# Kernel tuning notes

Hardware: AMD Instinct MI355X
Metric: run time of the kernel (lower is better)

Reference implementation:

```python
import jax, jax.numpy as jnp
import numpy as np


def setup_inputs() -> dict:
    key = jax.random.key(0)
    ks = jax.random.split(key, 16)
    s = 0.02
    return {
        "video": jax.random.normal(ks[0], (256, 10, 7, 7, 512), jnp.float32),
        "audio": jax.random.normal(ks[1], (10, 256, 128), jnp.float32),
        "Wv1": jax.random.normal(ks[2], (512, 512), jnp.float32) * s,
        "bv1": jnp.zeros((512,), jnp.float32),
        "Wa1": jax.random.normal(ks[3], (512, 128), jnp.float32) * s,
        "ba1": jnp.zeros((512,), jnp.float32),
        "Wb": jax.random.normal(ks[4], (256, 512), jnp.float32) * s,
        "bb": jnp.zeros((256,), jnp.float32),
        "Wc": jax.random.normal(ks[5], (512, 256), jnp.float32) * s,
        "bc": jnp.zeros((512,), jnp.float32),
        "Wv2": jax.random.normal(ks[6], (256, 512), jnp.float32) * s,
        "bv2": jnp.zeros((256,), jnp.float32),
        "Wa2": jax.random.normal(ks[7], (256, 128), jnp.float32) * s,
        "ba2": jnp.zeros((256,), jnp.float32),
        "Ws": jax.random.normal(ks[8], (1, 256), jnp.float32) * s,
        "bs": jnp.zeros((1,), jnp.float32),
    }


def reference(video, audio, Wv1, bv1, Wa1, ba1, Wb, bb, Wc, bc, Wv2, bv2, Wa2, ba2, Ws, bs):
    # video: [B, T, H, W, 512]; audio: [T, B, 128] (transposed inside, as in torch code)
    relu = jax.nn.relu
    audio = jnp.transpose(audio, (1, 0, 2))                  # [B, T, 128]
    B, T, H, W, Vd = video.shape
    BT, HW = B * T, H * W
    af = audio.reshape(BT, -1)                               # [BT, 128]
    vf = video.reshape(B, T, HW, Vd)                         # raw visual feature

    # channel attention
    aq1 = relu(af @ Wa1.T + ba1)[:, None, :]                 # [BT, 1, 512]
    vq1 = relu(vf @ Wv1.T + bv1).reshape(BT, HW, -1)         # [BT, 49, 512]
    avq = jnp.mean(aq1 * vq1, axis=-2)                       # [BT, 512]
    avq = relu(avq @ Wb.T + bb)                              # [BT, 256]
    c_att_maps = jax.nn.sigmoid(avq @ Wc.T + bc).reshape(B, T, 1, Vd)
    c_att = (vf * (c_att_maps + 1.0)).reshape(BT, HW, Vd)    # [BT, 49, 512]

    # spatial attention
    cq = relu(c_att @ Wv2.T + bv2)                           # [BT, 49, 256]
    aq2 = relu(af @ Wa2.T + ba2)[:, None, :]                 # [BT, 1, 256]
    logits = jnp.tanh((cq * aq2) @ Ws.T + bs)                # [BT, 49, 1]
    s_att = jax.nn.softmax(jnp.transpose(logits, (0, 2, 1)), axis=-1)  # [BT, 1, 49]

    out = jnp.matmul(s_att, c_att)                           # [BT, 1, 512]
    return out.reshape(B, T, Vd)
```

## Files before the change

### kernel.cpp

```cpp
#include <hip/hip_runtime.h>

typedef __bf16 bf16x8 __attribute__((ext_vector_type(8)));
typedef float f32x4 __attribute__((ext_vector_type(4)));

__device__ __forceinline__ unsigned short f2bf(float f) {
    union { float f; unsigned int u; } x; x.f = f;
    unsigned int r = x.u + 0x7FFFu + ((x.u >> 16) & 1u);
    return (unsigned short)(r >> 16);
}
__device__ __forceinline__ float bf2f(unsigned short v) {
    union { unsigned int u; float f; } x; x.u = ((unsigned int)v) << 16; return x.f;
}

__global__ __launch_bounds__(256) void k_prep(
    const float* __restrict__ Wv1, const float* __restrict__ Wv2,
    unsigned short* __restrict__ Wv1bf, unsigned short* __restrict__ Wv2bf)
{
    int idx = blockIdx.x * 256 + threadIdx.x;
    if (idx < 262144) {
        Wv1bf[idx] = f2bf(Wv1[idx]);
    } else {
        int j = idx - 262144;
        Wv2bf[j] = f2bf(Wv2[j]);
    }
}

__global__ __launch_bounds__(256) void k_audio(
    const float* __restrict__ audio,
    const float* __restrict__ Wa1, const float* __restrict__ ba1,
    const float* __restrict__ Wa2, const float* __restrict__ ba2,
    float* __restrict__ aq1, float* __restrict__ aq2)
{
    __shared__ float afs[4][128];
    const int btBase = blockIdx.x * 4;
    const int tid = threadIdx.x;
    for (int i = tid; i < 512; i += 256) {
        int g = i >> 7, k = i & 127;
        int bt = btBase + g;
        int b = bt / 10, t = bt - b * 10;
        afs[g][k] = audio[(t * 256 + b) * 128 + k];
    }
    __syncthreads();
    const int c = tid;
    float a1a[4] = {0.f,0.f,0.f,0.f}, a1b[4] = {0.f,0.f,0.f,0.f}, a2[4] = {0.f,0.f,0.f,0.f};
    const float* w1a = Wa1 + c * 128;
    const float* w1b = Wa1 + (c + 256) * 128;
    const float* w2p = Wa2 + c * 128;
    for (int kk = 0; kk < 32; ++kk) {
        float4 va = *(const float4*)(w1a + kk * 4);
        float4 vb = *(const float4*)(w1b + kk * 4);
        float4 vc = *(const float4*)(w2p + kk * 4);
        float fa[4] = {va.x, va.y, va.z, va.w};
        float fb[4] = {vb.x, vb.y, vb.z, vb.w};
        float fc[4] = {vc.x, vc.y, vc.z, vc.w};
#pragma unroll
        for (int j = 0; j < 4; ++j) {
            int k = kk * 4 + j;
#pragma unroll
            for (int g = 0; g < 4; ++g) {
                float a = afs[g][k];
                a1a[g] += a * fa[j];
                a1b[g] += a * fb[j];
                a2[g]  += a * fc[j];
            }
        }
    }
    float b1a = ba1[c], b1b = ba1[c + 256], b2 = ba2[c];
#pragma unroll
    for (int g = 0; g < 4; ++g) {
        int bt = btBase + g;
        aq1[bt * 512 + c]       = fmaxf(a1a[g] + b1a, 0.f);
        aq1[bt * 512 + c + 256] = fmaxf(a1b[g] + b1b, 0.f);
        aq2[bt * 256 + c]       = fmaxf(a2[g] + b2, 0.f);
    }
}

__global__ __launch_bounds__(256) void k_chanatt(
    const float* __restrict__ video,
    const unsigned short* __restrict__ Wv1bf, const float* __restrict__ bv1,
    const float* __restrict__ aq1, float* __restrict__ avq)
{
    __shared__ unsigned short At[49 * 512];
    const int bt = blockIdx.x;
    const int tid = threadIdx.x;
    const int wave = tid >> 6, lane = tid & 63, quad = lane >> 4, l16 = lane & 15;
    const float* vsrc = video + (size_t)bt * 25088;

    for (int c = tid; c < 3136; c += 256) {
        int row = c >> 6, ch = c & 63;
        float4 a = *(const float4*)(vsrc + row * 512 + ch * 8);
        float4 b = *(const float4*)(vsrc + row * 512 + ch * 8 + 4);
        float f[8] = {a.x, a.y, a.z, a.w, b.x, b.y, b.z, b.w};
        unsigned int o[8];
#pragma unroll
        for (int j = 0; j < 8; ++j) o[j] = f2bf(f[j]);
        uint4 pack;
        pack.x = o[0] | (o[1] << 16); pack.y = o[2] | (o[3] << 16);
        pack.z = o[4] | (o[5] << 16); pack.w = o[6] | (o[7] << 16);
        int chs = ch ^ (row & 7);
        *(uint4*)(&At[row * 512 + chs * 8]) = pack;
    }
    __syncthreads();

    f32x4 acc[4][8];
#pragma unroll
    for (int mt = 0; mt < 4; ++mt)
#pragma unroll
        for (int nt = 0; nt < 8; ++nt)
            acc[mt][nt] = (f32x4){0.f, 0.f, 0.f, 0.f};

    for (int kk = 0; kk < 16; ++kk) {
        int chunk = kk * 4 + quad;
        bf16x8 afrag[4];
#pragma unroll
        for (int mt = 0; mt < 4; ++mt) {
            int m = ((mt == 3) ? 33 : mt * 16) + l16;
            int chs = chunk ^ (m & 7);
            afrag[mt] = *(const bf16x8*)(&At[m * 512 + chs * 8]);
        }
        int koff = chunk * 8;
#pragma unroll
        for (int nt = 0; nt < 8; ++nt) {
            int n = (wave * 8 + nt) * 16 + l16;
            bf16x8 bfrag = *(const bf16x8*)(Wv1bf + n * 512 + koff);
#pragma unroll
            for (int mt = 0; mt < 4; ++mt)
                acc[mt][nt] = __builtin_amdgcn_mfma_f32_16x16x32_bf16(
                    afrag[mt], bfrag, acc[mt][nt], 0, 0, 0);
        }
    }

#pragma unroll
    for (int nt = 0; nt < 8; ++nt) {
        int n = (wave * 8 + nt) * 16 + l16;
        float bias = bv1[n];
        float s = 0.f;
#pragma unroll
        for (int mt = 0; mt < 4; ++mt)
#pragma unroll
            for (int r = 0; r < 4; ++r)
                if (mt < 3 || (quad == 3 && r == 3))
                    s += fmaxf(acc[mt][nt][r] + bias, 0.f);
        s += __shfl_xor(s, 16, 64);
        s += __shfl_xor(s, 32, 64);
        if (quad == 0) {
            float vm = s * (1.f / 49.f);
            avq[bt * 512 + n] = aq1[bt * 512 + n] * vm;
        }
    }
}

__global__ __launch_bounds__(256) void k_mlp(
    const float* __restrict__ avq,
    const float* __restrict__ Wb, const float* __restrict__ bb,
    const float* __restrict__ Wc, const float* __restrict__ bc,
    float* __restrict__ cmul)
{
    __shared__ float av[4][512];
    __shared__ float hid[4][256];
    const int btBase = blockIdx.x * 4;
    const int tid = threadIdx.x;
    for (int i = tid; i < 2048; i += 256) {
        int g = i >> 9, c = i & 511;
        av[g][c] = avq[(btBase + g) * 512 + c];
    }
    __syncthreads();
    {
        float a[4] = {0.f,0.f,0.f,0.f};
        const float* wrow = Wb + tid * 512;
        for (int kk = 0; kk < 128; ++kk) {
            float4 v = *(const float4*)(wrow + kk * 4);
            float w[4] = {v.x, v.y, v.z, v.w};
#pragma unroll
            for (int j = 0; j < 4; ++j)
#pragma unroll
                for (int g = 0; g < 4; ++g)
                    a[g] += av[g][kk * 4 + j] * w[j];
        }
        float bias = bb[tid];
#pragma unroll
        for (int g = 0; g < 4; ++g) hid[g][tid] = fmaxf(a[g] + bias, 0.f);
    }
    __syncthreads();
#pragma unroll
    for (int rep = 0; rep < 2; ++rep) {
        int c = tid + rep * 256;
        float a[4] = {0.f,0.f,0.f,0.f};
        const float* wrow = Wc + c * 256;
        for (int kk = 0; kk < 64; ++kk) {
            float4 v = *(const float4*)(wrow + kk * 4);
            float w[4] = {v.x, v.y, v.z, v.w};
#pragma unroll
            for (int j = 0; j < 4; ++j)
#pragma unroll
                for (int g = 0; g < 4; ++g)
                    a[g] += hid[g][kk * 4 + j] * w[j];
        }
        float bias = bc[c];
#pragma unroll
        for (int g = 0; g < 4; ++g) {
            float s = 1.f / (1.f + __expf(-(a[g] + bias)));
            cmul[(btBase + g) * 512 + c] = 1.f + s;
        }
    }
}

__global__ __launch_bounds__(256) void k_spatial(
    const float* __restrict__ video,
    const float* __restrict__ cmul, const float* __restrict__ aq2,
    const unsigned short* __restrict__ Wv2bf, const float* __restrict__ bv2,
    const float* __restrict__ Wsp, const float* __restrict__ bsp,
    float* __restrict__ out)
{
    __shared__ unsigned short Ct[49 * 512];
    __shared__ float w2[256];
    __shared__ float zbuf[4][64];
    __shared__ float smw[64];
    const int bt = blockIdx.x;
    const int tid = threadIdx.x;
    const int wave = tid >> 6, lane = tid & 63, quad = lane >> 4, l16 = lane & 15;
    const float* vsrc = video + (size_t)bt * 25088;
    const float* cm = cmul + bt * 512;

    for (int c = tid; c < 3136; c += 256) {
        int row = c >> 6, ch = c & 63;
        float4 a = *(const float4*)(vsrc + row * 512 + ch * 8);
        float4 b = *(const float4*)(vsrc + row * 512 + ch * 8 + 4);
        float f[8] = {a.x, a.y, a.z, a.w, b.x, b.y, b.z, b.w};
        float4 m0 = *(const float4*)(cm + ch * 8);
        float4 m1 = *(const float4*)(cm + ch * 8 + 4);
        float mm[8] = {m0.x, m0.y, m0.z, m0.w, m1.x, m1.y, m1.z, m1.w};
        unsigned int o[8];
#pragma unroll
        for (int j = 0; j < 8; ++j) o[j] = f2bf(f[j] * mm[j]);
        uint4 pack;
        pack.x = o[0] | (o[1] << 16); pack.y = o[2] | (o[3] << 16);
        pack.z = o[4] | (o[5] << 16); pack.w = o[6] | (o[7] << 16);
        int chs = ch ^ (row & 7);
        *(uint4*)(&Ct[row * 512 + chs * 8]) = pack;
    }
    w2[tid] = aq2[bt * 256 + tid] * Wsp[tid];
    if (lane >= 49) zbuf[wave][lane] = 0.f;
    __syncthreads();

    f32x4 acc[4][4];
#pragma unroll
    for (int mt = 0; mt < 4; ++mt)
#pragma unroll
        for (int nt = 0; nt < 4; ++nt)
            acc[mt][nt] = (f32x4){0.f, 0.f, 0.f, 0.f};

    for (int kk = 0; kk < 16; ++kk) {
        int chunk = kk * 4 + quad;
        bf16x8 afrag[4];
#pragma unroll
        for (int mt = 0; mt < 4; ++mt) {
            int m = ((mt == 3) ? 33 : mt * 16) + l16;
            int chs = chunk ^ (m & 7);
            afrag[mt] = *(const bf16x8*)(&Ct[m * 512 + chs * 8]);
        }
        int koff = chunk * 8;
#pragma unroll
        for (int nt = 0; nt < 4; ++nt) {
            int n = (wave * 4 + nt) * 16 + l16;
            bf16x8 bfrag = *(const bf16x8*)(Wv2bf + n * 512 + koff);
#pragma unroll
            for (int mt = 0; mt < 4; ++mt)
                acc[mt][nt] = __builtin_amdgcn_mfma_f32_16x16x32_bf16(
                    afrag[mt], bfrag, acc[mt][nt], 0, 0, 0);
        }
    }

    float zp[16];
#pragma unroll
    for (int i = 0; i < 16; ++i) zp[i] = 0.f;
#pragma unroll
    for (int nt = 0; nt < 4; ++nt) {
        int n = (wave * 4 + nt) * 16 + l16;
        float bias = bv2[n];
        float wn = w2[n];
#pragma unroll
        for (int mt = 0; mt < 4; ++mt)
#pragma unroll
            for (int r = 0; r < 4; ++r)
                zp[mt * 4 + r] += fmaxf(acc[mt][nt][r] + bias, 0.f) * wn;
    }
#pragma unroll
    for (int i = 0; i < 16; ++i) {
        float v = zp[i];
        v += __shfl_xor(v, 1, 64);
        v += __shfl_xor(v, 2, 64);
        v += __shfl_xor(v, 4, 64);
        v += __shfl_xor(v, 8, 64);
        zp[i] = v;
    }
    if (l16 == 0) {
#pragma unroll
        for (int mt = 0; mt < 4; ++mt)
#pragma unroll
            for (int r = 0; r < 4; ++r)
                if (mt < 3 || (quad == 3 && r == 3)) {
                    int row = ((mt == 3) ? 33 : mt * 16) + quad * 4 + r;
                    zbuf[wave][row] = zp[mt * 4 + r];
                }
    }
    __syncthreads();

    if (wave == 0) {
        int hw = lane;
        float z = zbuf[0][hw] + zbuf[1][hw] + zbuf[2][hw] + zbuf[3][hw] + bsp[0];
        float t = tanhf(z);
        float v = (hw < 49) ? t : -1e30f;
#pragma unroll
        for (int off = 32; off; off >>= 1) v = fmaxf(v, __shfl_xor(v, off, 64));
        float e = (hw < 49) ? __expf(t - v) : 0.f;
        float se = e;
#pragma unroll
        for (int off = 32; off; off >>= 1) se += __shfl_xor(se, off, 64);
        smw[hw] = e / se;
    }
    __syncthreads();

#pragma unroll
    for (int rep = 0; rep < 2; ++rep) {
        int cidx = tid + rep * 256;
        int chb = cidx >> 3, jj = cidx & 7;
        float s = 0.f;
        for (int hw = 0; hw < 49; ++hw) {
            int chs = chb ^ (hw & 7);
            s += smw[hw] * bf2f(Ct[hw * 512 + chs * 8 + jj]);
        }
        out[bt * 512 + cidx] = s;
    }
}

extern "C" void kernel_launch(void* const* d_in, const int* in_sizes, int n_in,
                              void* d_out, int out_size, void* d_ws, size_t ws_size,
                              hipStream_t stream) {
    const float* video = (const float*)d_in[0];
    const float* audio = (const float*)d_in[1];
    const float* Wv1 = (const float*)d_in[2];
    const float* bv1 = (const float*)d_in[3];
    const float* Wa1 = (const float*)d_in[4];
    const float* ba1 = (const float*)d_in[5];
    const float* Wb  = (const float*)d_in[6];
    const float* bb  = (const float*)d_in[7];
    const float* Wc  = (const float*)d_in[8];
    const float* bc  = (const float*)d_in[9];
    const float* Wv2 = (const float*)d_in[10];
    const float* bv2 = (const float*)d_in[11];
    const float* Wa2 = (const float*)d_in[12];
    const float* ba2 = (const float*)d_in[13];
    const float* Wsp = (const float*)d_in[14];
    const float* bsp = (const float*)d_in[15];

    float* ws = (float*)d_ws;
    float* aq1  = ws;
    float* aq2  = aq1 + 1310720;
    float* avq  = aq2 + 655360;
    float* cmul = avq + 1310720;
    unsigned short* Wv1bf = (unsigned short*)(cmul + 1310720);
    unsigned short* Wv2bf = Wv1bf + 262144;
    float* out = (float*)d_out;

    k_prep<<<1536, 256, 0, stream>>>(Wv1, Wv2, Wv1bf, Wv2bf);
    k_audio<<<640, 256, 0, stream>>>(audio, Wa1, ba1, Wa2, ba2, aq1, aq2);
    k_chanatt<<<2560, 256, 0, stream>>>(video, Wv1bf, bv1, aq1, avq);
    k_mlp<<<640, 256, 0, stream>>>(avq, Wb, bb, Wc, bc, cmul);
    k_spatial<<<2560, 256, 0, stream>>>(video, cmul, aq2, Wv2bf, bv2, Wsp, bsp, out);
}
```

Baseline: 815.3 us.

## Pre-convert video to bf16 and stage tiles into LDS with async loads

Adds a pass that converts the whole video tensor to bf16 once in workspace. The channel-attention and spatial kernels then load their tiles directly into swizzled LDS with global_load_lds instead of loading fp32 and converting per block. The spatial kernel applies the channel-attention scale in place in LDS using packed bf16 conversion. This removes the redundant fp32 reads and conversions but adds a full extra read/write pass and needs a large workspace, with a fallback to the old kernels otherwise.

```diff
diff --git a/kernel.cpp b/kernel.cpp
--- a/kernel.cpp
+++ b/kernel.cpp
@@ -10,6 +10,22 @@
 }
 __device__ __forceinline__ float bf2f(unsigned short v) {
     union { unsigned int u; float f; } x; x.u = ((unsigned int)v) << 16; return x.f;
+}
+__device__ __forceinline__ float bf2f_lo(unsigned int w) {
+    union { unsigned int u; float f; } x; x.u = w << 16; return x.f;
+}
+__device__ __forceinline__ float bf2f_hi(unsigned int w) {
+    union { unsigned int u; float f; } x; x.u = w & 0xffff0000u; return x.f;
+}
+__device__ __forceinline__ unsigned int cvt_pk_bf16(float lo, float hi) {
+    unsigned int r;
+    asm("v_cvt_pk_bf16_f32 %0, %1, %2" : "=v"(r) : "v"(lo), "v"(hi));
+    return r;
+}
+__device__ __forceinline__ void async16(const void* g, void* l) {
+    __builtin_amdgcn_global_load_lds(
+        (const __attribute__((address_space(1))) unsigned int*)g,
+        (__attribute__((address_space(3))) unsigned int*)l, 16, 0, 0);
 }
 
 __global__ __launch_bounds__(256) void k_prep(
@@ -22,6 +38,21 @@
     } else {
         int j = idx - 262144;
         Wv2bf[j] = f2bf(Wv2[j]);
+    }
+}
+
+__global__ __launch_bounds__(256) void k_prepv(
+    const float* __restrict__ v, unsigned short* __restrict__ vbf)
+{
+    const size_t stride = (size_t)gridDim.x * 256;
+    for (size_t c = (size_t)blockIdx.x * 256 + threadIdx.x; c < 8028160u; c += stride) {
+        const float* p = v + c * 8;
+        float4 a = *(const float4*)p;
+        float4 b = *(const float4*)(p + 4);
+        uint4 o;
+        o.x = cvt_pk_bf16(a.x, a.y); o.y = cvt_pk_bf16(a.z, a.w);
+        o.z = cvt_pk_bf16(b.x, b.y); o.w = cvt_pk_bf16(b.z, b.w);
+        *(uint4*)(vbf + c * 8) = o;
     }
 }
 
@@ -76,6 +107,278 @@
 }
 
 __global__ __launch_bounds__(256) void k_chanatt(
+    const unsigned short* __restrict__ videobf,
+    const unsigned short* __restrict__ Wv1bf, const float* __restrict__ bv1,
+    const float* __restrict__ aq1, float* __restrict__ avq)
+{
+    __shared__ unsigned short At[49 * 512];
+    const int bt = blockIdx.x;
+    const int tid = threadIdx.x;
+    const int wave = tid >> 6, lane = tid & 63, quad = lane >> 4, l16 = lane & 15;
+    const unsigned short* vsrc = videobf + (size_t)bt * 25088;
+
+#pragma unroll
+    for (int i = 0; i < 13; ++i) {
+        int p = i * 256 + tid;
+        if (p < 3136) {
+            int row = p >> 6;
+            int ch = (p & 63) ^ (row & 7);
+            async16(vsrc + row * 512 + ch * 8, &At[p * 8]);
+        }
+    }
+    __syncthreads();
+
+#pragma unroll 1
+    for (int npass = 0; npass < 2; ++npass) {
+        f32x4 acc[4][4];
+#pragma unroll
+        for (int mt = 0; mt < 4; ++mt)
+#pragma unroll
+            for (int nt = 0; nt < 4; ++nt)
+                acc[mt][nt] = (f32x4){0.f, 0.f, 0.f, 0.f};
+
+        for (int kk = 0; kk < 16; ++kk) {
+            int chunk = kk * 4 + quad;
+            bf16x8 afrag[4];
+#pragma unroll
+            for (int mt = 0; mt < 4; ++mt) {
+                int m = ((mt == 3) ? 33 : mt * 16) + l16;
+                int chs = chunk ^ (m & 7);
+                afrag[mt] = *(const bf16x8*)(&At[m * 512 + chs * 8]);
+            }
+            int koff = chunk * 8;
+#pragma unroll
+            for (int nt = 0; nt < 4; ++nt) {
+                int n = (wave * 8 + npass * 4 + nt) * 16 + l16;
+                bf16x8 bfrag = *(const bf16x8*)(Wv1bf + n * 512 + koff);
+#pragma unroll
+                for (int mt = 0; mt < 4; ++mt)
+                    acc[mt][nt] = __builtin_amdgcn_mfma_f32_16x16x32_bf16(
+                        afrag[mt], bfrag, acc[mt][nt], 0, 0, 0);
+            }
+        }
+
+#pragma unroll
+        for (int nt = 0; nt < 4; ++nt) {
+            int n = (wave * 8 + npass * 4 + nt) * 16 + l16;
+            float bias = bv1[n];
+            float s = 0.f;
+#pragma unroll
+            for (int mt = 0; mt < 4; ++mt)
+#pragma unroll
+                for (int r = 0; r < 4; ++r)
+                    if (mt < 3 || (quad == 3 && r == 3))
+                        s += fmaxf(acc[mt][nt][r] + bias, 0.f);
+            s += __shfl_xor(s, 16, 64);
+            s += __shfl_xor(s, 32, 64);
+            if (quad == 0) {
+                float vm = s * (1.f / 49.f);
+                avq[bt * 512 + n] = aq1[bt * 512 + n] * vm;
+            }
+        }
+    }
+}
+
+__global__ __launch_bounds__(256) void k_mlp(
+    const float* __restrict__ avq,
+    const float* __restrict__ Wb, const float* __restrict__ bb,
+    const float* __restrict__ Wc, const float* __restrict__ bc,
+    float* __restrict__ cmul)
+{
+    __shared__ float av[4][512];
+    __shared__ float hid[4][256];
+    const int btBase = blockIdx.x * 4;
+    const int tid = threadIdx.x;
+    for (int i = tid; i < 2048; i += 256) {
+        int g = i >> 9, c = i & 511;
+        av[g][c] = avq[(btBase + g) * 512 + c];
+    }
+    __syncthreads();
+    {
+        float a[4] = {0.f,0.f,0.f,0.f};
+        const float* wrow = Wb + tid * 512;
+        for (int kk = 0; kk < 128; ++kk) {
+            float4 v = *(const float4*)(wrow + kk * 4);
+            float w[4] = {v.x, v.y, v.z, v.w};
+#pragma unroll
+            for (int j = 0; j < 4; ++j)
+#pragma unroll
+                for (int g = 0; g < 4; ++g)
+                    a[g] += av[g][kk * 4 + j] * w[j];
+        }
+        float bias = bb[tid];
+#pragma unroll
+        for (int g = 0; g < 4; ++g) hid[g][tid] = fmaxf(a[g] + bias, 0.f);
+    }
+    __syncthreads();
+#pragma unroll
+    for (int rep = 0; rep < 2; ++rep) {
+        int c = tid + rep * 256;
+        float a[4] = {0.f,0.f,0.f,0.f};
+        const float* wrow = Wc + c * 256;
+        for (int kk = 0; kk < 64; ++kk) {
+            float4 v = *(const float4*)(wrow + kk * 4);
+            float w[4] = {v.x, v.y, v.z, v.w};
+#pragma unroll
+            for (int j = 0; j < 4; ++j)
+#pragma unroll
+                for (int g = 0; g < 4; ++g)
+                    a[g] += hid[g][kk * 4 + j] * w[j];
+        }
+        float bias = bc[c];
+#pragma unroll
+        for (int g = 0; g < 4; ++g) {
+            float s = 1.f / (1.f + __expf(-(a[g] + bias)));
+            cmul[(btBase + g) * 512 + c] = 1.f + s;
+        }
+    }
+}
+
+__global__ __launch_bounds__(256) void k_spatial(
+    const unsigned short* __restrict__ videobf,
+    const float* __restrict__ cmul, const float* __restrict__ aq2,
+    const unsigned short* __restrict__ Wv2bf, const float* __restrict__ bv2,
+    const float* __restrict__ Wsp, const float* __restrict__ bsp,
+    float* __restrict__ out)
+{
+    __shared__ unsigned short Ct[49 * 512];
+    __shared__ float w2[256];
+    __shared__ float zbuf[4][64];
+    __shared__ float smw[64];
+    const int bt = blockIdx.x;
+    const int tid = threadIdx.x;
+    const int wave = tid >> 6, lane = tid & 63, quad = lane >> 4, l16 = lane & 15;
+    const unsigned short* vsrc = videobf + (size_t)bt * 25088;
+
+#pragma unroll
+    for (int i = 0; i < 13; ++i) {
+        int p = i * 256 + tid;
+        if (p < 3136) {
+            int row = p >> 6;
+            int ch = (p & 63) ^ (row & 7);
+            async16(vsrc + row * 512 + ch * 8, &Ct[p * 8]);
+        }
+    }
+    w2[tid] = aq2[bt * 256 + tid] * Wsp[tid];
+    if (lane >= 49) zbuf[wave][lane] = 0.f;
+    const int ch0 = tid & 63, rg = tid >> 6;
+    float cmv[8];
+    {
+        const float* cmp = cmul + bt * 512 + ch0 * 8;
+        float4 c0 = *(const float4*)cmp;
+        float4 c1 = *(const float4*)(cmp + 4);
+        cmv[0]=c0.x; cmv[1]=c0.y; cmv[2]=c0.z; cmv[3]=c0.w;
+        cmv[4]=c1.x; cmv[5]=c1.y; cmv[6]=c1.z; cmv[7]=c1.w;
+    }
+    __syncthreads();
+
+#pragma unroll
+    for (int row = rg; row < 49; row += 4) {
+        int chs = ch0 ^ (row & 7);
+        uint4* p = (uint4*)(&Ct[row * 512 + chs * 8]);
+        uint4 v = *p;
+        unsigned int w[4] = {v.x, v.y, v.z, v.w};
+        uint4 o;
+        o.x = cvt_pk_bf16(bf2f_lo(w[0]) * cmv[0], bf2f_hi(w[0]) * cmv[1]);
+        o.y = cvt_pk_bf16(bf2f_lo(w[1]) * cmv[2], bf2f_hi(w[1]) * cmv[3]);
+        o.z = cvt_pk_bf16(bf2f_lo(w[2]) * cmv[4], bf2f_hi(w[2]) * cmv[5]);
+        o.w = cvt_pk_bf16(bf2f_lo(w[3]) * cmv[6], bf2f_hi(w[3]) * cmv[7]);
+        *p = o;
+    }
+    __syncthreads();
+
+    f32x4 acc[4][4];
+#pragma unroll
+    for (int mt = 0; mt < 4; ++mt)
+#pragma unroll
+        for (int nt = 0; nt < 4; ++nt)
+            acc[mt][nt] = (f32x4){0.f, 0.f, 0.f, 0.f};
+
+    for (int kk = 0; kk < 16; ++kk) {
+        int chunk = kk * 4 + quad;
+        bf16x8 afrag[4];
+#pragma unroll
+        for (int mt = 0; mt < 4; ++mt) {
+            int m = ((mt == 3) ? 33 : mt * 16) + l16;
+            int chs = chunk ^ (m & 7);
+            afrag[mt] = *(const bf16x8*)(&Ct[m * 512 + chs * 8]);
+        }
+        int koff = chunk * 8;
+#pragma unroll
+        for (int nt = 0; nt < 4; ++nt) {
+            int n = (wave * 4 + nt) * 16 + l16;
+            bf16x8 bfrag = *(const bf16x8*)(Wv2bf + n * 512 + koff);
+#pragma unroll
+            for (int mt = 0; mt < 4; ++mt)
+                acc[mt][nt] = __builtin_amdgcn_mfma_f32_16x16x32_bf16(
+                    afrag[mt], bfrag, acc[mt][nt], 0, 0, 0);
+        }
+    }
+
+    float zp[16];
+#pragma unroll
+    for (int i = 0; i < 16; ++i) zp[i] = 0.f;
+#pragma unroll
+    for (int nt = 0; nt < 4; ++nt) {
+        int n = (wave * 4 + nt) * 16 + l16;
+        float bias = bv2[n];
+        float wn = w2[n];
+#pragma unroll
+        for (int mt = 0; mt < 4; ++mt)
+#pragma unroll
+            for (int r = 0; r < 4; ++r)
+                zp[mt * 4 + r] += fmaxf(acc[mt][nt][r] + bias, 0.f) * wn;
+    }
+#pragma unroll
+    for (int i = 0; i < 16; ++i) {
+        float v = zp[i];
+        v += __shfl_xor(v, 1, 64);
+        v += __shfl_xor(v, 2, 64);
+        v += __shfl_xor(v, 4, 64);
+        v += __shfl_xor(v, 8, 64);
+        zp[i] = v;
+    }
+    if (l16 == 0) {
+#pragma unroll
+        for (int mt = 0; mt < 4; ++mt)
+#pragma unroll
+            for (int r = 0; r < 4; ++r)
+                if (mt < 3 || (quad == 3 && r == 3)) {
+                    int row = ((mt == 3) ? 33 : mt * 16) + quad * 4 + r;
+                    zbuf[wave][row] = zp[mt * 4 + r];
+                }
+    }
+    __syncthreads();
+
+    if (wave == 0) {
+        int hw = lane;
+        float z = zbuf[0][hw] + zbuf[1][hw] + zbuf[2][hw] + zbuf[3][hw] + bsp[0];
+        float t = tanhf(z);
+        float v = (hw < 49) ? t : -1e30f;
+#pragma unroll
+        for (int off = 32; off; off >>= 1) v = fmaxf(v, __shfl_xor(v, off, 64));
+        float e = (hw < 49) ? __expf(t - v) : 0.f;
+        float se = e;
+#pragma unroll
+        for (int off = 32; off; off >>= 1) se += __shfl_xor(se, off, 64);
+        smw[hw] = e / se;
+    }
+    __syncthreads();
+
+#pragma unroll
+    for (int rep = 0; rep < 2; ++rep) {
+        int cidx = tid + rep * 256;
+        int chb = cidx >> 3, jj = cidx & 7;
+        float s = 0.f;
+        for (int hw = 0; hw < 49; ++hw) {
+            int chs = chb ^ (hw & 7);
+            s += smw[hw] * bf2f(Ct[hw * 512 + chs * 8 + jj]);
+        }
+        out[bt * 512 + cidx] = s;
+    }
+}
+
+__global__ __launch_bounds__(256) void k_chanatt_fb(
     const float* __restrict__ video,
     const unsigned short* __restrict__ Wv1bf, const float* __restrict__ bv1,
     const float* __restrict__ aq1, float* __restrict__ avq)
@@ -150,62 +453,7 @@
     }
 }
 
-__global__ __launch_bounds__(256) void k_mlp(
-    const float* __restrict__ avq,
-    const float* __restrict__ Wb, const float* __restrict__ bb,
-    const float* __restrict__ Wc, const float* __restrict__ bc,
-    float* __restrict__ cmul)
-{
-    __shared__ float av[4][512];
-    __shared__ float hid[4][256];
-    const int btBase = blockIdx.x * 4;
-    const int tid = threadIdx.x;
-    for (int i = tid; i < 2048; i += 256) {
-        int g = i >> 9, c = i & 511;
-        av[g][c] = avq[(btBase + g) * 512 + c];
-    }
-    __syncthreads();
-    {
-        float a[4] = {0.f,0.f,0.f,0.f};
-        const float* wrow = Wb + tid * 512;
-        for (int kk = 0; kk < 128; ++kk) {
-            float4 v = *(const float4*)(wrow + kk * 4);
-            float w[4] = {v.x, v.y, v.z, v.w};
-#pragma unroll
-            for (int j = 0; j < 4; ++j)
-#pragma unroll
-                for (int g = 0; g < 4; ++g)
-                    a[g] += av[g][kk * 4 + j] * w[j];
-        }
-        float bias = bb[tid];
-#pragma unroll
-        for (int g = 0; g < 4; ++g) hid[g][tid] = fmaxf(a[g] + bias, 0.f);
-    }
-    __syncthreads();
-#pragma unroll
-    for (int rep = 0; rep < 2; ++rep) {
-        int c = tid + rep * 256;
-        float a[4] = {0.f,0.f,0.f,0.f};
-        const float* wrow = Wc + c * 256;
-        for (int kk = 0; kk < 64; ++kk) {
-            float4 v = *(const float4*)(wrow + kk * 4);
-            float w[4] = {v.x, v.y, v.z, v.w};
-#pragma unroll
-            for (int j = 0; j < 4; ++j)
-#pragma unroll
-                for (int g = 0; g < 4; ++g)
-                    a[g] += hid[g][kk * 4 + j] * w[j];
-        }
-        float bias = bc[c];
-#pragma unroll
-        for (int g = 0; g < 4; ++g) {
-            float s = 1.f / (1.f + __expf(-(a[g] + bias)));
-            cmul[(btBase + g) * 512 + c] = 1.f + s;
-        }
-    }
-}
-
-__global__ __launch_bounds__(256) void k_spatial(
+__global__ __launch_bounds__(256) void k_spatial_fb(
     const float* __restrict__ video,
     const float* __restrict__ cmul, const float* __restrict__ aq2,
     const unsigned short* __restrict__ Wv2bf, const float* __restrict__ bv2,
@@ -353,19 +601,38 @@
     const float* ba2 = (const float*)d_in[13];
     const float* Wsp = (const float*)d_in[14];
     const float* bsp = (const float*)d_in[15];
-
-    float* ws = (float*)d_ws;
-    float* aq1  = ws;
-    float* aq2  = aq1 + 1310720;
-    float* avq  = aq2 + 655360;
-    float* cmul = avq + 1310720;
-    unsigned short* Wv1bf = (unsigned short*)(cmul + 1310720);
-    unsigned short* Wv2bf = Wv1bf + 262144;
     float* out = (float*)d_out;
 
-    k_prep<<<1536, 256, 0, stream>>>(Wv1, Wv2, Wv1bf, Wv2bf);
-    k_audio<<<640, 256, 0, stream>>>(audio, Wa1, ba1, Wa2, ba2, aq1, aq2);
-    k_chanatt<<<2560, 256, 0, stream>>>(video, Wv1bf, bv1, aq1, avq);
-    k_mlp<<<640, 256, 0, stream>>>(avq, Wb, bb, Wc, bc, cmul);
-    k_spatial<<<2560, 256, 0, stream>>>(video, cmul, aq2, Wv2bf, bv2, Wsp, bsp, out);
-}
+    const size_t NEED = 147587072u;
+    if (ws_size >= NEED) {
+        unsigned short* videobf = (unsigned short*)d_ws;
+        unsigned short* Wv1bf = videobf + 64225280;
+        unsigned short* Wv2bf = Wv1bf + 262144;
+        float* fbase = (float*)(Wv2bf + 131072);
+        float* aq1  = fbase;
+        float* aq2  = aq1 + 1310720;
+        float* avq  = aq2 + 655360;
+        float* cmul = avq + 1310720;
+
+        k_prep<<<1536, 256, 0, stream>>>(Wv1, Wv2, Wv1bf, Wv2bf);
+        k_audio<<<640, 256, 0, stream>>>(audio, Wa1, ba1, Wa2, ba2, aq1, aq2);
+        k_prepv<<<4096, 256, 0, stream>>>(video, videobf);
+        k_chanatt<<<2560, 256, 0, stream>>>(videobf, Wv1bf, bv1, aq1, avq);
+        k_mlp<<<640, 256, 0, stream>>>(avq, Wb, bb, Wc, bc, cmul);
+        k_spatial<<<2560, 256, 0, stream>>>(videobf, cmul, aq2, Wv2bf, bv2, Wsp, bsp, out);
+    } else {
+        float* ws = (float*)d_ws;
+        float* aq1  = ws;
+        float* aq2  = aq1 + 1310720;
+        float* avq  = aq2 + 655360;
+        float* cmul = avq + 1310720;
+        unsigned short* Wv1bf = (unsigned short*)(cmul + 1310720);
+        unsigned short* Wv2bf = Wv1bf + 262144;
+
+        k_prep<<<1536, 256, 0, stream>>>(Wv1, Wv2, Wv1bf, Wv2bf);
+        k_audio<<<640, 256, 0, stream>>>(audio, Wa1, ba1, Wa2, ba2, aq1, aq2);
+        k_chanatt_fb<<<2560, 256, 0, stream>>>(video, Wv1bf, bv1, aq1, avq);
+        k_mlp<<<640, 256, 0, stream>>>(avq, Wb, bb, Wc, bc, cmul);
+        k_spatial_fb<<<2560, 256, 0, stream>>>(video, cmul, aq2, Wv2bf, bv2, Wsp, bsp, out);
+    }
+}
```

New measurement: 908.8 us. +11.5%, slower.
